# Kernel tuning notes

Measured on AMD Instinct MI355X. Metric: run time of the kernel, lower is better.

The kernel has to match this reference:

```python
import jax, jax.numpy as jnp
import numpy as np

D_MODEL = 1024
NUM_HEADS = 16
D_K = D_MODEL // NUM_HEADS
B, L = 2, 4096


def setup_inputs() -> dict:
    key = jax.random.key(0)
    ks = jax.random.split(key, 12)
    s = 0.02
    return {
        "q": jax.random.normal(ks[0], (B, L, D_MODEL), dtype=jnp.float32),
        "k": jax.random.normal(ks[1], (B, L, D_MODEL), dtype=jnp.float32),
        "v": jax.random.normal(ks[2], (B, L, D_MODEL), dtype=jnp.float32),
        "Wq": jax.random.normal(ks[3], (D_MODEL, D_MODEL), dtype=jnp.float32) * s,
        "bq": jax.random.normal(ks[4], (D_MODEL,), dtype=jnp.float32) * s,
        "Wk": jax.random.normal(ks[5], (D_MODEL, D_MODEL), dtype=jnp.float32) * s,
        "bk": jax.random.normal(ks[6], (D_MODEL,), dtype=jnp.float32) * s,
        "Wv": jax.random.normal(ks[7], (D_MODEL, D_MODEL), dtype=jnp.float32) * s,
        "bv": jax.random.normal(ks[8], (D_MODEL,), dtype=jnp.float32) * s,
        "Wo": jax.random.normal(ks[9], (D_MODEL, D_MODEL), dtype=jnp.float32) * s,
        "bo": jax.random.normal(ks[10], (D_MODEL,), dtype=jnp.float32) * s,
    }


def reference(q, k, v, Wq, bq, Wk, bk, Wv, bv, Wo, bo):
    b, l, _ = q.shape
    # projections (torch Linear: x @ W.T + b), reshape to [b, l, h, d]
    qf = (q @ Wq.T + bq).reshape(b, l, NUM_HEADS, D_K)
    kf = (k @ Wk.T + bk).reshape(b, l, NUM_HEADS, D_K)
    vf = (v @ Wv.T + bv).reshape(b, l, NUM_HEADS, D_K)
    # elu+1 feature map (positive features)
    qf = jax.nn.elu(qf) + 1.0
    kf = jax.nn.elu(kf) + 1.0
    # normalizer uses full-sequence k sum (as in the original code)
    z = 1.0 / (jnp.einsum("blhd,bhd->blh", qf, kf.sum(axis=1)) + 1e-6)
    # cumulative sums over sequence (the linear-attention scan state)
    k_cum = jnp.cumsum(kf, axis=1)  # [b, l, h, d]
    v_cum = jnp.cumsum(vf, axis=1)  # [b, l, h, d]
    context = jnp.einsum("blhd,blhd->blh", qf, k_cum)  # [b, l, h]
    context = context[..., None] * v_cum * z[..., None]  # [b, l, h, d]
    context = context.reshape(b, l, NUM_HEADS * D_K)
    return context @ Wo.T + bo
```

## Files before the change

### kernel.cpp

```cpp
#include <hip/hip_runtime.h>
#include <hip/hip_bf16.h>
#include <cstdint>
#include <cstddef>

#define D_MODEL 1024
#define NUM_HEADS 16
#define DK_DIM 64
#define BATCH 2
#define SEQ 4096
#define MROWS (BATCH*SEQ)
#define NCHUNK 128
#define CHUNK 32

#define BM 256
#define BN 128
#define BK 64
#define NSLOT 3
#define SLOT_SH (BM*BK + BN*BK)
#define KTILES (D_MODEL/BK)

typedef __attribute__((ext_vector_type(4))) float f32x4;
typedef __attribute__((ext_vector_type(2))) float f32x2;
typedef __attribute__((ext_vector_type(8))) short bf16x8;
typedef __attribute__((ext_vector_type(4))) short s16x4;
typedef __attribute__((ext_vector_type(2))) uint32_t u32x2;
typedef __attribute__((ext_vector_type(4))) uint32_t u32x4;

__device__ __forceinline__ float b2f(short s) {
  union { uint32_t u; float f; } c; c.u = ((uint32_t)(uint16_t)s) << 16; return c.f;
}
__device__ __forceinline__ short f2b(float f) {
  union { float f; uint32_t u; } c; c.f = f;
  uint32_t u = c.u;
  u += 0x7FFFu + ((u >> 16) & 1u);
  return (short)(u >> 16);
}
__device__ __forceinline__ f32x4 b4_to_f4(s16x4 s) {
  f32x4 r;
  r.x = b2f(s.x); r.y = b2f(s.y); r.z = b2f(s.z); r.w = b2f(s.w);
  return r;
}
__device__ __forceinline__ uint32_t cvtpk(float lo, float hi) {
  uint32_t r;
  asm("v_cvt_pk_bf16_f32 %0, %1, %2" : "=v"(r) : "v"(lo), "v"(hi));
  return r;
}

__global__ __launch_bounds__(256) void cvt_w4(
    const float* __restrict__ s0, const float* __restrict__ s1,
    const float* __restrict__ s2, const float* __restrict__ s3,
    short* __restrict__ dst) {
  const int y = blockIdx.y;
  const float* s = (y == 0) ? s0 : (y == 1) ? s1 : (y == 2) ? s2 : s3;
  const int i = blockIdx.x * 256 + threadIdx.x;
  float4 v = reinterpret_cast<const float4*>(s)[i];
  s16x4 o;
  o.x = f2b(v.x); o.y = f2b(v.y); o.z = f2b(v.z); o.w = f2b(v.w);
  reinterpret_cast<s16x4*>(dst)[(size_t)y * (D_MODEL * D_MODEL / 4) + i] = o;
}

template<int AFP32, int OUTBF16>
__global__ __launch_bounds__(512, 2) void gemm8(
    const void* __restrict__ Ap, const short* __restrict__ Bw,
    const float* __restrict__ bias, void* __restrict__ Cout, int act)
{
  extern __shared__ __align__(16) short lds[];
  const int tid = threadIdx.x;
  const int wid = tid >> 6;
  const int lane = tid & 63;
  const int brow = blockIdx.x * BM;
  const int bcol = blockIdx.y * BN;
  const int wr = wid >> 1, wc = wid & 1;
  const float* __restrict__ A32 = (const float*)Ap;
  const short* __restrict__ A16 = (const short*)Ap;

  f32x4 acc[4][4];
#pragma unroll
  for (int i = 0; i < 4; ++i)
#pragma unroll
    for (int j = 0; j < 4; ++j)
#pragma unroll
      for (int t = 0; t < 4; ++t) acc[i][j][t] = 0.f;

  const int srow = lane >> 3;
  const int gql  = lane & 7;
  const int sgel = (gql ^ srow) * 8;

  auto stageB = [&](int t) {
    short* sB = lds + (t % NSLOT) * SLOT_SH + BM * BK;
    const int k0 = t * BK;
#pragma unroll
    for (int i = 0; i < 2; ++i) {
      const int r = i * 64 + wid * 8;
      const short* g = Bw + (size_t)(bcol + r + srow) * D_MODEL + k0 + sgel;
      __builtin_amdgcn_global_load_lds((const __attribute__((address_space(1))) void*)g,
          (__attribute__((address_space(3))) void*)(sB + r * BK), 16, 0, 0);
    }
  };
  auto stageA16 = [&](int t) {
    short* sA = lds + (t % NSLOT) * SLOT_SH;
    const int k0 = t * BK;
#pragma unroll
    for (int i = 0; i < 4; ++i) {
      const int r = i * 64 + wid * 8;
      const short* g = A16 + (size_t)(brow + r + srow) * D_MODEL + k0 + sgel;
      __builtin_amdgcn_global_load_lds((const __attribute__((address_space(1))) void*)g,
          (__attribute__((address_space(3))) void*)(sA + r * BK), 16, 0, 0);
    }
  };
  auto loadA32 = [&](int t, float4 (&buf)[8]) {
    const int k0 = t * BK;
#pragma unroll
    for (int i = 0; i < 4; ++i) {
      const float* src = A32 + (size_t)(brow + i * 64 + wid * 8 + srow) * D_MODEL + k0 + gql * 8;
      buf[2 * i]     = *reinterpret_cast<const float4*>(src);
      buf[2 * i + 1] = *reinterpret_cast<const float4*>(src + 4);
    }
  };
  auto writeA32 = [&](int t, float4 (&buf)[8]) {
    char* sA = (char*)(lds + (t % NSLOT) * SLOT_SH);
#pragma unroll
    for (int i = 0; i < 4; ++i) {
      u32x4 w;
      w.x = cvtpk(buf[2 * i].x,     buf[2 * i].y);
      w.y = cvtpk(buf[2 * i].z,     buf[2 * i].w);
      w.z = cvtpk(buf[2 * i + 1].x, buf[2 * i + 1].y);
      w.w = cvtpk(buf[2 * i + 1].z, buf[2 * i + 1].w);
      const int ebyte = (i * 64 + wid * 8 + srow) * 128 + ((gql ^ srow) * 16);
      *reinterpret_cast<u32x4*>(sA + ebyte) = w;
    }
  };

  const int lane15 = lane & 15;
  const int swz = (lane & 7) << 4;
  const int kq = (lane >> 4) * 16;

  auto compute = [&](int t) {
    const char* sAb = (const char*)(lds + (t % NSLOT) * SLOT_SH);
    const char* sBb = sAb + BM * BK * 2;
    auto rdA = [&](int mi, int ks) -> bf16x8 {
      const int row = wr * 64 + mi * 16 + lane15;
      const int off = row * 128 + ((ks * 64 + kq) ^ swz);
      return *reinterpret_cast<const bf16x8*>(sAb + off);
    };
    auto rdB = [&](int nj, int ks) -> bf16x8 {
      const int row = wc * 64 + nj * 16 + lane15;
      const int off = row * 128 + ((ks * 64 + kq) ^ swz);
      return *reinterpret_cast<const bf16x8*>(sBb + off);
    };
    bf16x8 Af[2][2], Bf[2][2][2];
#pragma unroll
    for (int m2 = 0; m2 < 2; ++m2)
#pragma unroll
      for (int ks = 0; ks < 2; ++ks) Af[m2][ks] = rdA(m2, ks);
#pragma unroll
    for (int j2 = 0; j2 < 2; ++j2)
#pragma unroll
      for (int ks = 0; ks < 2; ++ks) Bf[0][j2][ks] = rdB(j2, ks);
    __builtin_amdgcn_s_setprio(1);
#pragma unroll
    for (int m2 = 0; m2 < 2; ++m2)
#pragma unroll
      for (int j2 = 0; j2 < 2; ++j2)
#pragma unroll
        for (int ks = 0; ks < 2; ++ks)
          acc[m2][j2] = __builtin_amdgcn_mfma_f32_16x16x32_bf16(Bf[0][j2][ks], Af[m2][ks], acc[m2][j2], 0, 0, 0);
    __builtin_amdgcn_s_setprio(0);
    __builtin_amdgcn_sched_barrier(0);
#pragma unroll
    for (int j2 = 0; j2 < 2; ++j2)
#pragma unroll
      for (int ks = 0; ks < 2; ++ks) Bf[1][j2][ks] = rdB(2 + j2, ks);
    __builtin_amdgcn_s_setprio(1);
#pragma unroll
    for (int m2 = 0; m2 < 2; ++m2)
#pragma unroll
      for (int j2 = 0; j2 < 2; ++j2)
#pragma unroll
        for (int ks = 0; ks < 2; ++ks)
          acc[m2][2 + j2] = __builtin_amdgcn_mfma_f32_16x16x32_bf16(Bf[1][j2][ks], Af[m2][ks], acc[m2][2 + j2], 0, 0, 0);
    __builtin_amdgcn_s_setprio(0);
    __builtin_amdgcn_sched_barrier(0);
#pragma unroll
    for (int m2 = 0; m2 < 2; ++m2)
#pragma unroll
      for (int ks = 0; ks < 2; ++ks) Af[m2][ks] = rdA(2 + m2, ks);
    __builtin_amdgcn_s_setprio(1);
#pragma unroll
    for (int m2 = 0; m2 < 2; ++m2)
#pragma unroll
      for (int j2 = 0; j2 < 2; ++j2)
#pragma unroll
        for (int ks = 0; ks < 2; ++ks)
          acc[2 + m2][2 + j2] = __builtin_amdgcn_mfma_f32_16x16x32_bf16(Bf[1][j2][ks], Af[m2][ks], acc[2 + m2][2 + j2], 0, 0, 0);
    __builtin_amdgcn_s_setprio(0);
    __builtin_amdgcn_sched_barrier(0);
    __builtin_amdgcn_s_setprio(1);
#pragma unroll
    for (int m2 = 0; m2 < 2; ++m2)
#pragma unroll
      for (int j2 = 0; j2 < 2; ++j2)
#pragma unroll
        for (int ks = 0; ks < 2; ++ks)
          acc[2 + m2][j2] = __builtin_amdgcn_mfma_f32_16x16x32_bf16(Bf[0][j2][ks], Af[m2][ks], acc[2 + m2][j2], 0, 0, 0);
    __builtin_amdgcn_s_setprio(0);
    __builtin_amdgcn_sched_barrier(0);
  };

  if constexpr (AFP32) {
    float4 buf0[8], buf1[8];
    loadA32(0, buf0);
    asm volatile("s_waitcnt vmcnt(0)" ::: "memory");
    writeA32(0, buf0);
    loadA32(1, buf1);
    stageB(0); stageB(1);

    auto body = [&](int t, float4 (&bufW)[8], float4 (&bufL)[8]) {
      if (t == KTILES - 1) { asm volatile("s_waitcnt vmcnt(0)" ::: "memory"); }
      else                 { asm volatile("s_waitcnt vmcnt(2)" ::: "memory"); }
      if (t + 1 < KTILES) writeA32(t + 1, bufW);
      if (t + 2 < KTILES) loadA32(t + 2, bufL);
      asm volatile("s_waitcnt lgkmcnt(0)" ::: "memory");
      __builtin_amdgcn_s_barrier();
      __builtin_amdgcn_sched_barrier(0);
      if (t + 2 < KTILES) stageB(t + 2);
      compute(t);
    };
#pragma unroll 1
    for (int t2 = 0; t2 < KTILES; t2 += 2) {
      body(t2,     buf1, buf0);
      body(t2 + 1, buf0, buf1);
    }
  } else {
    stageA16(0); stageB(0);
    stageA16(1); stageB(1);
#pragma unroll 1
    for (int t = 0; t < KTILES; ++t) {
      if (t == KTILES - 1) { asm volatile("s_waitcnt vmcnt(0)" ::: "memory"); }
      else                 { asm volatile("s_waitcnt vmcnt(6)" ::: "memory"); }
      __builtin_amdgcn_s_barrier();
      __builtin_amdgcn_sched_barrier(0);
      if (t + 2 < KTILES) { stageA16(t + 2); stageB(t + 2); }
      compute(t);
    }
  }

  const int csub4 = (lane >> 4) * 4;
#pragma unroll
  for (int mi = 0; mi < 4; ++mi) {
    const int row = brow + wr * 64 + mi * 16 + lane15;
    const size_t rowbase = (size_t)row * D_MODEL;
#pragma unroll
    for (int nj = 0; nj < 4; ++nj) {
      const int col0 = bcol + wc * 64 + nj * 16 + csub4;
      const float4 bv = *reinterpret_cast<const float4*>(&bias[col0]);
      float v0 = acc[mi][nj][0] + bv.x;
      float v1 = acc[mi][nj][1] + bv.y;
      float v2 = acc[mi][nj][2] + bv.z;
      float v3 = acc[mi][nj][3] + bv.w;
      if (act) {
        v0 = (v0 > 0.f) ? (v0 + 1.f) : __expf(v0);
        v1 = (v1 > 0.f) ? (v1 + 1.f) : __expf(v1);
        v2 = (v2 > 0.f) ? (v2 + 1.f) : __expf(v2);
        v3 = (v3 > 0.f) ? (v3 + 1.f) : __expf(v3);
      }
      if (OUTBF16) {
        u32x2 w;
        w.x = cvtpk(v0, v1);
        w.y = cvtpk(v2, v3);
        *reinterpret_cast<u32x2*>(&((short*)Cout)[rowbase + col0]) = w;
      } else {
        float4 w; w.x = v0; w.y = v1; w.z = v2; w.w = v3;
        *reinterpret_cast<float4*>(&((float*)Cout)[rowbase + col0]) = w;
      }
    }
  }
}

__global__ __launch_bounds__(256) void chunk_sums(
    const short* __restrict__ kf, const short* __restrict__ vf,
    float* __restrict__ ck, float* __restrict__ cv)
{
  const int gw = blockIdx.x * 4 + (threadIdx.x >> 6);
  const int lane = threadIdx.x & 63;
  const int c = gw & (NCHUNK - 1);
  const int h = (gw >> 7) & (NUM_HEADS - 1);
  const int b = gw >> 11;
  const int half = lane >> 5;
  const int dpair = (lane & 31) * 2;
  const size_t base = ((size_t)(b * SEQ + c * CHUNK) * NUM_HEADS + h) * DK_DIM + dpair;

  float skx = 0.f, sky = 0.f, svx = 0.f, svy = 0.f;
#pragma unroll
  for (int i = 0; i < CHUNK / 2; ++i) {
    const size_t off = base + (size_t)(2 * i + half) * D_MODEL;
    uint32_t ku = *reinterpret_cast<const uint32_t*>(&kf[off]);
    uint32_t vu = *reinterpret_cast<const uint32_t*>(&vf[off]);
    skx += b2f((short)(ku & 0xffff)); sky += b2f((short)(ku >> 16));
    svx += b2f((short)(vu & 0xffff)); svy += b2f((short)(vu >> 16));
  }
  skx += __shfl_xor(skx, 32, 64); sky += __shfl_xor(sky, 32, 64);
  svx += __shfl_xor(svx, 32, 64); svy += __shfl_xor(svy, 32, 64);
  if (half == 0) {
    const size_t o = ((size_t)((b * NUM_HEADS + h) * NCHUNK + c)) * DK_DIM + dpair;
    f32x2 a; a.x = skx; a.y = sky;
    f32x2 bb; bb.x = svx; bb.y = svy;
    *reinterpret_cast<f32x2*>(&ck[o]) = a;
    *reinterpret_cast<f32x2*>(&cv[o]) = bb;
  }
}

__global__ __launch_bounds__(64) void chunk_scan(
    float* __restrict__ ck, float* __restrict__ cv, float* __restrict__ ksum)
{
  const int bh = blockIdx.x;
  const int d = threadIdx.x;
  float rk = 0.f, rv = 0.f;
#pragma unroll 8
  for (int c = 0; c < NCHUNK; ++c) {
    const size_t o = ((size_t)(bh * NCHUNK + c)) * DK_DIM + d;
    const float tk = ck[o], tv = cv[o];
    ck[o] = rk; cv[o] = rv;
    rk += tk; rv += tv;
  }
  ksum[bh * DK_DIM + d] = rk;
}

__global__ __launch_bounds__(256) void scan_ctx(
    const short* __restrict__ qf, const short* __restrict__ kf,
    const short* __restrict__ vf,
    const float* __restrict__ ck, const float* __restrict__ cv,
    const float* __restrict__ ksum, short* __restrict__ ctx)
{
  const int gw = blockIdx.x * 4 + (threadIdx.x >> 6);
  const int lane = threadIdx.x & 63;
  const int pg = lane >> 4;
  const int dg = lane & 15;
  const int c = gw & (NCHUNK - 1);
  const int h = (gw >> 7) & (NUM_HEADS - 1);
  const int b = gw >> 11;
  const int bh = b * NUM_HEADS + h;
  const int d4 = dg * 4;

  f32x4 krun = *reinterpret_cast<const f32x4*>(
      &ck[((size_t)(bh * NCHUNK + c)) * DK_DIM + d4]);
  f32x4 vrun = *reinterpret_cast<const f32x4*>(
      &cv[((size_t)(bh * NCHUNK + c)) * DK_DIM + d4]);
  const f32x4 kst = *reinterpret_cast<const f32x4*>(&ksum[bh * DK_DIM + d4]);

  const size_t base = ((size_t)(b * SEQ + c * CHUNK) * NUM_HEADS + h) * DK_DIM + d4;

  for (int p0 = 0; p0 < CHUNK; p0 += 4) {
    const size_t qoff = base + (size_t)(p0 + pg) * D_MODEL;
    const f32x4 q4 = b4_to_f4(*reinterpret_cast<const s16x4*>(&qf[qoff]));
    f32x4 sk, sv;
#pragma unroll
    for (int i = 0; i < 4; ++i) {
      const size_t off = base + (size_t)(p0 + i) * D_MODEL;
      krun += b4_to_f4(*reinterpret_cast<const s16x4*>(&kf[off]));
      vrun += b4_to_f4(*reinterpret_cast<const s16x4*>(&vf[off]));
      if (i == pg) { sk = krun; sv = vrun; }
    }
    float s1 = q4.x * sk.x + q4.y * sk.y + q4.z * sk.z + q4.w * sk.w;
    float s2 = q4.x * kst.x + q4.y * kst.y + q4.z * kst.z + q4.w * kst.w;
#pragma unroll
    for (int m = 1; m < 16; m <<= 1) {
      s1 += __shfl_xor(s1, m, 64);
      s2 += __shfl_xor(s2, m, 64);
    }
    const float g = s1 / (s2 + 1e-6f);
    s16x4 o;
    o.x = f2b(g * sv.x); o.y = f2b(g * sv.y);
    o.z = f2b(g * sv.z); o.w = f2b(g * sv.w);
    *reinterpret_cast<s16x4*>(&ctx[qoff]) = o;
  }
}

extern "C" void kernel_launch(void* const* d_in, const int* in_sizes, int n_in,
                              void* d_out, int out_size, void* d_ws, size_t ws_size,
                              hipStream_t stream) {
  const float* q  = (const float*)d_in[0];
  const float* k  = (const float*)d_in[1];
  const float* v  = (const float*)d_in[2];
  const float* Wq = (const float*)d_in[3];
  const float* bq = (const float*)d_in[4];
  const float* Wk = (const float*)d_in[5];
  const float* bk = (const float*)d_in[6];
  const float* Wv = (const float*)d_in[7];
  const float* bv = (const float*)d_in[8];
  const float* Wo = (const float*)d_in[9];
  const float* bo = (const float*)d_in[10];
  float* out = (float*)d_out;

  uint8_t* p = (uint8_t*)d_ws;
  auto alloc = [&](size_t bytes) { uint8_t* r = p; p += bytes; return r; };
  short* qf  = (short*)alloc((size_t)MROWS * D_MODEL * 2);
  short* kf  = (short*)alloc((size_t)MROWS * D_MODEL * 2);
  short* vf  = (short*)alloc((size_t)MROWS * D_MODEL * 2);
  short* ctx = (short*)alloc((size_t)MROWS * D_MODEL * 2);
  short* Wqb = (short*)alloc((size_t)D_MODEL * D_MODEL * 2);
  short* Wkb = (short*)alloc((size_t)D_MODEL * D_MODEL * 2);
  short* Wvb = (short*)alloc((size_t)D_MODEL * D_MODEL * 2);
  short* Wob = (short*)alloc((size_t)D_MODEL * D_MODEL * 2);
  float* ck   = (float*)alloc((size_t)BATCH * NUM_HEADS * NCHUNK * DK_DIM * 4);
  float* cv   = (float*)alloc((size_t)BATCH * NUM_HEADS * NCHUNK * DK_DIM * 4);
  float* ksum = (float*)alloc((size_t)BATCH * NUM_HEADS * DK_DIM * 4);

  const dim3 ggrid(MROWS / BM, D_MODEL / BN);
  const int shbytes = NSLOT * SLOT_SH * (int)sizeof(short);

  (void)hipFuncSetAttribute((const void*)gemm8<1, 1>,
      hipFuncAttributeMaxDynamicSharedMemorySize, shbytes);
  (void)hipFuncSetAttribute((const void*)gemm8<0, 0>,
      hipFuncAttributeMaxDynamicSharedMemorySize, shbytes);

  cvt_w4<<<dim3(D_MODEL * D_MODEL / 4 / 256, 4), 256, 0, stream>>>(Wq, Wk, Wv, Wo, Wqb);

  gemm8<1, 1><<<ggrid, 512, shbytes, stream>>>(q, Wqb, bq, qf, 1);
  gemm8<1, 1><<<ggrid, 512, shbytes, stream>>>(k, Wkb, bk, kf, 1);
  gemm8<1, 1><<<ggrid, 512, shbytes, stream>>>(v, Wvb, bv, vf, 0);

  chunk_sums<<<BATCH * NUM_HEADS * NCHUNK / 4, 256, 0, stream>>>(kf, vf, ck, cv);
  chunk_scan<<<BATCH * NUM_HEADS, 64, 0, stream>>>(ck, cv, ksum);
  scan_ctx<<<BATCH * NUM_HEADS * NCHUNK / 4, 256, 0, stream>>>(qf, kf, vf, ck, cv, ksum, ctx);

  gemm8<0, 0><<<ggrid, 512, shbytes, stream>>>(ctx, Wob, bo, out, 0);
}
```

Measured before the change: 144.3 us.

## Batch Q/K/V projections into one grid launch and drop MFMA priority hints

The three separate projection GEMM launches are merged into a single launch with a z-dimension of 3. Each z-slice selects its own input, bias, weight slice and output slab, relying on the contiguous workspace layout of qf/kf/vf and Wq/Wk/Wv. This removes two launch boundaries and tail effects, letting blocks from all three projections fill the GPU together. Separately, the s_setprio and sched_barrier hints around the MFMA groups are removed, which hands instruction scheduling back to the compiler and may change how LDS reads interleave with MFMAs.

```diff
diff --git a/kernel.cpp b/kernel.cpp
--- a/kernel.cpp
+++ b/kernel.cpp
@@ -61,8 +61,10 @@
 
 template<int AFP32, int OUTBF16>
 __global__ __launch_bounds__(512, 2) void gemm8(
-    const void* __restrict__ Ap, const short* __restrict__ Bw,
-    const float* __restrict__ bias, void* __restrict__ Cout, int act)
+    const void* __restrict__ A0, const void* __restrict__ A1,
+    const void* __restrict__ A2, const short* __restrict__ Wbase,
+    const float* __restrict__ b0, const float* __restrict__ b1,
+    const float* __restrict__ b2, void* __restrict__ Cbase, int actmask)
 {
   extern __shared__ __align__(16) short lds[];
   const int tid = threadIdx.x;
@@ -70,7 +72,13 @@
   const int lane = tid & 63;
   const int brow = blockIdx.x * BM;
   const int bcol = blockIdx.y * BN;
+  const int z = blockIdx.z;
   const int wr = wid >> 1, wc = wid & 1;
+
+  const void* Ap = (z == 0) ? A0 : (z == 1) ? A1 : A2;
+  const float* bias = (z == 0) ? b0 : (z == 1) ? b1 : b2;
+  const short* Bw = Wbase + (size_t)z * D_MODEL * D_MODEL;
+  const int act = (actmask >> z) & 1;
   const float* __restrict__ A32 = (const float*)Ap;
   const short* __restrict__ A16 = (const short*)Ap;
 
@@ -157,7 +165,6 @@
     for (int j2 = 0; j2 < 2; ++j2)
 #pragma unroll
       for (int ks = 0; ks < 2; ++ks) Bf[0][j2][ks] = rdB(j2, ks);
-    __builtin_amdgcn_s_setprio(1);
 #pragma unroll
     for (int m2 = 0; m2 < 2; ++m2)
 #pragma unroll
@@ -165,13 +172,10 @@
 #pragma unroll
         for (int ks = 0; ks < 2; ++ks)
           acc[m2][j2] = __builtin_amdgcn_mfma_f32_16x16x32_bf16(Bf[0][j2][ks], Af[m2][ks], acc[m2][j2], 0, 0, 0);
-    __builtin_amdgcn_s_setprio(0);
-    __builtin_amdgcn_sched_barrier(0);
 #pragma unroll
     for (int j2 = 0; j2 < 2; ++j2)
 #pragma unroll
       for (int ks = 0; ks < 2; ++ks) Bf[1][j2][ks] = rdB(2 + j2, ks);
-    __builtin_amdgcn_s_setprio(1);
 #pragma unroll
     for (int m2 = 0; m2 < 2; ++m2)
 #pragma unroll
@@ -179,13 +183,10 @@
 #pragma unroll
         for (int ks = 0; ks < 2; ++ks)
           acc[m2][2 + j2] = __builtin_amdgcn_mfma_f32_16x16x32_bf16(Bf[1][j2][ks], Af[m2][ks], acc[m2][2 + j2], 0, 0, 0);
-    __builtin_amdgcn_s_setprio(0);
-    __builtin_amdgcn_sched_barrier(0);
 #pragma unroll
     for (int m2 = 0; m2 < 2; ++m2)
 #pragma unroll
       for (int ks = 0; ks < 2; ++ks) Af[m2][ks] = rdA(2 + m2, ks);
-    __builtin_amdgcn_s_setprio(1);
 #pragma unroll
     for (int m2 = 0; m2 < 2; ++m2)
 #pragma unroll
@@ -193,9 +194,6 @@
 #pragma unroll
         for (int ks = 0; ks < 2; ++ks)
           acc[2 + m2][2 + j2] = __builtin_amdgcn_mfma_f32_16x16x32_bf16(Bf[1][j2][ks], Af[m2][ks], acc[2 + m2][2 + j2], 0, 0, 0);
-    __builtin_amdgcn_s_setprio(0);
-    __builtin_amdgcn_sched_barrier(0);
-    __builtin_amdgcn_s_setprio(1);
 #pragma unroll
     for (int m2 = 0; m2 < 2; ++m2)
 #pragma unroll
@@ -203,8 +201,6 @@
 #pragma unroll
         for (int ks = 0; ks < 2; ++ks)
           acc[2 + m2][j2] = __builtin_amdgcn_mfma_f32_16x16x32_bf16(Bf[0][j2][ks], Af[m2][ks], acc[2 + m2][j2], 0, 0, 0);
-    __builtin_amdgcn_s_setprio(0);
-    __builtin_amdgcn_sched_barrier(0);
   };
 
   if constexpr (AFP32) {
@@ -249,7 +245,7 @@
 #pragma unroll
   for (int mi = 0; mi < 4; ++mi) {
     const int row = brow + wr * 64 + mi * 16 + lane15;
-    const size_t rowbase = (size_t)row * D_MODEL;
+    const size_t rowbase = (size_t)z * MROWS * D_MODEL + (size_t)row * D_MODEL;
 #pragma unroll
     for (int nj = 0; nj < 4; ++nj) {
       const int col0 = bcol + wc * 64 + nj * 16 + csub4;
@@ -268,10 +264,10 @@
         u32x2 w;
         w.x = cvtpk(v0, v1);
         w.y = cvtpk(v2, v3);
-        *reinterpret_cast<u32x2*>(&((short*)Cout)[rowbase + col0]) = w;
+        *reinterpret_cast<u32x2*>(&((short*)Cbase)[rowbase + col0]) = w;
       } else {
         float4 w; w.x = v0; w.y = v1; w.z = v2; w.w = v3;
-        *reinterpret_cast<float4*>(&((float*)Cout)[rowbase + col0]) = w;
+        *reinterpret_cast<float4*>(&((float*)Cbase)[rowbase + col0]) = w;
       }
     }
   }
@@ -405,8 +401,10 @@
   float* ck   = (float*)alloc((size_t)BATCH * NUM_HEADS * NCHUNK * DK_DIM * 4);
   float* cv   = (float*)alloc((size_t)BATCH * NUM_HEADS * NCHUNK * DK_DIM * 4);
   float* ksum = (float*)alloc((size_t)BATCH * NUM_HEADS * DK_DIM * 4);
-
-  const dim3 ggrid(MROWS / BM, D_MODEL / BN);
+  (void)Wkb; (void)Wvb;
+
+  const dim3 gproj(MROWS / BM, D_MODEL / BN, 3);
+  const dim3 gout (MROWS / BM, D_MODEL / BN, 1);
   const int shbytes = NSLOT * SLOT_SH * (int)sizeof(short);
 
   (void)hipFuncSetAttribute((const void*)gemm8<1, 1>,
@@ -416,13 +414,11 @@
 
   cvt_w4<<<dim3(D_MODEL * D_MODEL / 4 / 256, 4), 256, 0, stream>>>(Wq, Wk, Wv, Wo, Wqb);
 
-  gemm8<1, 1><<<ggrid, 512, shbytes, stream>>>(q, Wqb, bq, qf, 1);
-  gemm8<1, 1><<<ggrid, 512, shbytes, stream>>>(k, Wkb, bk, kf, 1);
-  gemm8<1, 1><<<ggrid, 512, shbytes, stream>>>(v, Wvb, bv, vf, 0);
+  gemm8<1, 1><<<gproj, 512, shbytes, stream>>>(q, k, v, Wqb, bq, bk, bv, qf, 0x3);
 
   chunk_sums<<<BATCH * NUM_HEADS * NCHUNK / 4, 256, 0, stream>>>(kf, vf, ck, cv);
   chunk_scan<<<BATCH * NUM_HEADS, 64, 0, stream>>>(ck, cv, ksum);
   scan_ctx<<<BATCH * NUM_HEADS * NCHUNK / 4, 256, 0, stream>>>(qf, kf, vf, ck, cv, ksum, ctx);
 
-  gemm8<0, 0><<<ggrid, 512, shbytes, stream>>>(ctx, Wob, bo, out, 0);
-}
+  gemm8<0, 0><<<gout, 512, shbytes, stream>>>(ctx, ctx, ctx, Wob, bo, bo, bo, out, 0);
+}
```

Result: faster. 140.8 us (-2.4%).
